# Performance work log

Hardware: AMD Instinct MI355X
Metric: run time of the kernel (lower is better)

Reference implementation:

```python
import jax, jax.numpy as jnp
import numpy as np

LOG2 = float(np.log(2.0))

def ssp(x):
    # shifted softplus: log(0.5*exp(x) + 0.5)
    return jax.nn.softplus(x) - LOG2


def setup_inputs() -> dict:
    B, A, N = 8, 512, 64
    n_atom, n_spatial, n_filters = 256, 128, 256
    n_ang_feat = 2 * 2 * 2 * 8 * 2  # 2*n_zetas*2*n_angular*n_zetas = 128
    key = jax.random.key(0)
    ks = jax.random.split(key, 16)
    f32 = jnp.float32
    inp = {
        'x': jax.random.normal(ks[0], (B, A, n_atom), f32),
        'r_ij': jax.random.uniform(ks[1], (B, A, N), f32) * 6.0,  # some beyond cutoff=5
        'f_ij': jax.random.normal(ks[2], (B, A, N, n_spatial), f32),
        'G_i': jax.random.normal(ks[3], (B, A, n_ang_feat), f32),
        'neighbor_mask': jnp.ones((B, A, N), f32),
        'neighbors': jax.random.randint(ks[4], (B, A, N), 0, A),
        # CFConv params: in2f (no bias), filter MLP, f2out
        'W_in2f': jax.random.normal(ks[5], (n_atom, n_filters), f32) * (n_atom ** -0.5),
        'W1': jax.random.normal(ks[6], (n_spatial, n_filters), f32) * (n_spatial ** -0.5),
        'b1': jnp.zeros((n_filters,), f32),
        'W2': jax.random.normal(ks[7], (n_filters, n_filters), f32) * (n_filters ** -0.5),
        'b2': jnp.zeros((n_filters,), f32),
        'W_f2out': jax.random.normal(ks[8], (n_filters, n_atom), f32) * (n_filters ** -0.5),
        'b_f2out': jnp.zeros((n_atom,), f32),
        # post-cfconv dense and angular dense (no bias)
        'W_dense': jax.random.normal(ks[9], (n_atom, n_atom), f32) * (n_atom ** -0.5),
        'b_dense': jnp.zeros((n_atom,), f32),
        'W_ang': jax.random.normal(ks[10], (n_ang_feat, n_atom), f32) * (n_ang_feat ** -0.5),
    }
    return inp


def reference(x, r_ij, f_ij, G_i, neighbor_mask, neighbors,
              W_in2f, W1, b1, W2, b2, W_f2out, b_f2out,
              W_dense, b_dense, W_ang):
    cutoff = 5.0
    # filter-generating MLP on distance expansion: [B,A,N,n_filters]
    W = ssp(jnp.einsum('bans,sf->banf', f_ij, W1) + b1)
    W = jnp.einsum('banf,fg->bang', W, W2) + b2
    # hard cutoff mask on distances
    C = (r_ij <= cutoff).astype(W.dtype)
    W = W * C[..., None]
    # in2f projection then neighbor gather
    xf = jnp.einsum('bad,df->baf', x, W_in2f)  # [B,A,F]
    B, A, F = xf.shape
    N = neighbors.shape[-1]
    y = jnp.take_along_axis(xf, neighbors.reshape(B, A * N, 1), axis=1)
    y = y.reshape(B, A, N, F)
    # elementwise filter, mask padded neighbors, sum-aggregate over neighbors
    y = (y * W * neighbor_mask[..., None]).sum(axis=2)  # [B,A,F]
    v_rad = jnp.einsum('baf,fd->bad', y, W_f2out) + b_f2out
    v_rad = jnp.einsum('bad,de->bae', v_rad, W_dense) + b_dense
    v_ang = jnp.einsum('bag,gd->bad', G_i, W_ang)
    return ssp(v_rad + v_ang)
```

## Files before the change

kernel.cpp:

```cpp
#include <hip/hip_runtime.h>


typedef __bf16 bf16x8 __attribute__((ext_vector_type(8)));
typedef float f32x4 __attribute__((ext_vector_type(4)));
typedef unsigned short u16;
typedef unsigned int u32;

#define LDA 136
#define LDH 264

__device__ __forceinline__ float b2f(u16 u) {
  union { float f; u32 i; } v; v.i = ((u32)u) << 16; return v.f;
}
__device__ __forceinline__ u32 rndb(float f) {
  u32 u = __builtin_bit_cast(u32, f);
  return u + 0x7fffu + ((u >> 16) & 1u);
}
__device__ __forceinline__ u16 f2b(float f) { return (u16)(rndb(f) >> 16); }
__device__ __forceinline__ u32 pkbf(float lo, float hi) {
  return __builtin_amdgcn_perm(rndb(hi), rndb(lo), 0x07060302);
}
__device__ __forceinline__ float sspf(float x) {
  float t = __expf(-fabsf(x));
  return fmaxf(x, 0.0f) + __logf(1.0f + t) - 0.6931471805599453f;
}
__device__ __forceinline__ bf16x8 ldfrag(const u16* p) {
  return __builtin_bit_cast(bf16x8, *(const uint4*)p);
}
__device__ __forceinline__ float ldsc(const u16* p, bool fm, size_t i) {
  return fm ? ((const float*)p)[i] : b2f(p[i]);
}
__device__ __forceinline__ void cvt8_store(u16* dst, const float* s) {
  float4 a = *(const float4*)s, b = *(const float4*)(s + 4);
  uint4 r;
  r.x = pkbf(a.x, a.y); r.y = pkbf(a.z, a.w);
  r.z = pkbf(b.x, b.y); r.w = pkbf(b.z, b.w);
  *(uint4*)dst = r;
}
__device__ __forceinline__ bf16x8 ldfragW_bf(const u16* W, int k0, int col, int quad) {
  union { u16 s[8]; bf16x8 v; } r;
#pragma unroll
  for (int j = 0; j < 8; j++) r.s[j] = W[(size_t)(k0 + quad * 8 + j) * 256 + col];
  return r.v;
}

__device__ __forceinline__ void pack_chunk(const u16* W, bool fm, int ksh, int idx, u16* dst) {
  int flane = idx & 63;
  int q = (idx >> 6) & ((1 << ksh) - 1);
  int c = idx >> (6 + ksh);
  int row = q * 32 + (flane >> 4) * 8;
  int col = c * 16 + (flane & 15);
  uint4 r;
  if (fm) {
    const float* p = (const float*)W + (size_t)row * 256 + col;
    r.x = pkbf(p[0], p[256]);   r.y = pkbf(p[512], p[768]);
    r.z = pkbf(p[1024], p[1280]); r.w = pkbf(p[1536], p[1792]);
  } else {
    const u16* p = W + (size_t)row * 256 + col;
    r.x = (u32)p[0] | ((u32)p[256] << 16);
    r.y = (u32)p[512] | ((u32)p[768] << 16);
    r.z = (u32)p[1024] | ((u32)p[1280] << 16);
    r.w = (u32)p[1536] | ((u32)p[1792] << 16);
  }
  *(uint4*)(dst + (size_t)idx * 8) = r;
}

__global__ __launch_bounds__(256) void pack_win(
    const u16* __restrict__ Win, const u16* __restrict__ nm, u16* __restrict__ outb) {
  if (nm[0] != 0) return;
  int g = blockIdx.x * 256 + threadIdx.x;
  pack_chunk(Win, true, 3, g, outb + 1048576);
}

__global__ __launch_bounds__(256) void pack5(
    const u16* __restrict__ W1, const u16* __restrict__ W2, const u16* __restrict__ Wf,
    const u16* __restrict__ Wd, const u16* __restrict__ Wa,
    const u16* __restrict__ nm, u16* __restrict__ dst) {
  bool fm = (nm[0] == 0);
  int g = blockIdx.x * 256 + threadIdx.x;
  if (g < 4096)        pack_chunk(W1, fm, 2, g, dst);
  else if (g < 12288)  pack_chunk(W2, fm, 3, g - 4096, dst + 32768);
  else if (g < 20480)  pack_chunk(Wf, fm, 3, g - 12288, dst + 98304);
  else if (g < 28672)  pack_chunk(Wd, fm, 3, g - 20480, dst + 163840);
  else                 pack_chunk(Wa, fm, 2, g - 28672, dst + 229376);
}

__global__ __launch_bounds__(256) void k1_xf(
    const u16* __restrict__ x, const u16* __restrict__ Win,
    const u16* __restrict__ nm, u16* __restrict__ outb) {
  __shared__ __align__(16) u16 sX[16 * LDH];
  bool fm = (nm[0] == 0);
  int bid = blockIdx.x, tid = threadIdx.x;
  int w = tid >> 6, lane = tid & 63, quad = lane >> 4, l16 = lane & 15;
  if (fm) {
    const float* src = (const float*)x + (size_t)bid * 4096;
#pragma unroll
    for (int i = 0; i < 2; i++) {
      int c = tid + 256 * i;
      cvt8_store(sX + (c >> 5) * LDH + (c & 31) * 8, src + c * 8);
    }
  } else {
    const u16* src = x + (size_t)bid * 4096;
#pragma unroll
    for (int i = 0; i < 2; i++) {
      int c = tid + 256 * i;
      *(uint4*)(sX + (c >> 5) * LDH + (c & 31) * 8) = *(const uint4*)(src + c * 8);
    }
  }
  __syncthreads();
  const u16* winp = outb + 1048576;
  f32x4 acc[4];
#pragma unroll
  for (int ct = 0; ct < 4; ct++) acc[ct] = (f32x4){0.f, 0.f, 0.f, 0.f};
#pragma unroll
  for (int q = 0; q < 8; q++) {
    bf16x8 af = ldfrag(sX + l16 * LDH + q * 32 + quad * 8);
    bf16x8 bfr[4];
#pragma unroll
    for (int ct = 0; ct < 4; ct++)
      bfr[ct] = fm ? ldfrag(winp + ((size_t)((w * 4 + ct) * 8 + q) * 64 + lane) * 8)
                   : ldfragW_bf(Win, q * 32, (w * 4 + ct) * 16 + l16, quad);
#pragma unroll
    for (int ct = 0; ct < 4; ct++)
      acc[ct] = __builtin_amdgcn_mfma_f32_16x16x32_bf16(af, bfr[ct], acc[ct], 0, 0, 0);
  }
#pragma unroll
  for (int ct = 0; ct < 4; ct++) {
    int f = w * 64 + ct * 16 + l16;
#pragma unroll
    for (int r = 0; r < 4; r++)
      outb[(size_t)(bid * 16 + quad * 4 + r) * 256 + f] = f2b(acc[ct][r]);
  }
}

__global__ __launch_bounds__(256, 3) void k2_main(
    u16* __restrict__ fij, const u16* __restrict__ rij, const u16* __restrict__ nm,
    const int* __restrict__ nbr, const u16* __restrict__ b1, const u16* __restrict__ b2,
    const u16* __restrict__ packed, const u16* __restrict__ xf) {
  __shared__ __align__(16) u16 sF[64 * LDA];
  __shared__ __align__(16) u16 sH[64 * LDH];
  __shared__ float cm[64];
  __shared__ int nb[64];
  bool fm = (nm[0] == 0);
  const u16* w1p = packed;
  const u16* w2p = packed + 32768;
  int bid = blockIdx.x, tid = threadIdx.x;
  int w = tid >> 6, lane = tid & 63, quad = lane >> 4, l16 = lane & 15;

  if (fm) {
    const float* fsrc = (const float*)fij + (size_t)bid * 8192;
#pragma unroll
    for (int i = 0; i < 4; i++) {
      int c = tid + 256 * i;
      cvt8_store(sF + (c >> 4) * LDA + (c & 15) * 8, fsrc + c * 8);
    }
  } else {
    const u16* fsrc = fij + (size_t)bid * 8192;
#pragma unroll
    for (int i = 0; i < 4; i++) {
      int c = tid + 256 * i;
      *(uint4*)(sF + (c >> 4) * LDA + (c & 15) * 8) = *(const uint4*)(fsrc + c * 8);
    }
  }
  if (tid < 64) {
    float r = ldsc(rij, fm, (size_t)bid * 64 + tid);
    float m = ldsc(nm, fm, (size_t)bid * 64 + tid);
    cm[tid] = (r <= 5.0f) ? m : 0.0f;
    nb[tid] = nbr[bid * 64 + tid];
  }
  __syncthreads();

  int b_of = (bid >> 9) * 512;
  u32 xr[4][4][2];
#pragma unroll
  for (int mt = 0; mt < 4; mt++)
#pragma unroll
    for (int r = 0; r < 4; r++) {
      int m = mt * 16 + quad * 4 + r;
      const u16* src = xf + ((size_t)(b_of + nb[m])) * 256 + w * 64 + l16;
      u32 t0 = src[0], t1 = src[16], t2 = src[32], t3 = src[48];
      xr[mt][r][0] = t0 | (t1 << 16);
      xr[mt][r][1] = t2 | (t3 << 16);
    }

  f32x4 zero = {0.f, 0.f, 0.f, 0.f};
  f32x4 acc[4][4];
#pragma unroll
  for (int mt = 0; mt < 4; mt++)
#pragma unroll
    for (int ct = 0; ct < 4; ct++) acc[mt][ct] = zero;
#pragma unroll
  for (int q = 0; q < 4; q++) {
    bf16x8 af[4], bfr[4];
#pragma unroll
    for (int mt = 0; mt < 4; mt++)
      af[mt] = ldfrag(sF + (mt * 16 + l16) * LDA + q * 32 + quad * 8);
#pragma unroll
    for (int ct = 0; ct < 4; ct++)
      bfr[ct] = ldfrag(w1p + ((size_t)((w * 4 + ct) * 4 + q) * 64 + lane) * 8);
#pragma unroll
    for (int mt = 0; mt < 4; mt++)
#pragma unroll
      for (int ct = 0; ct < 4; ct++)
        acc[mt][ct] = __builtin_amdgcn_mfma_f32_16x16x32_bf16(af[mt], bfr[ct], acc[mt][ct], 0, 0, 0);
  }
#pragma unroll
  for (int ct = 0; ct < 4; ct++) {
    int f = w * 64 + ct * 16 + l16;
    float bb = ldsc(b1, fm, f);
#pragma unroll
    for (int mt = 0; mt < 4; mt++)
#pragma unroll
      for (int r = 0; r < 4; r++)
        sH[(mt * 16 + quad * 4 + r) * LDH + f] = f2b(sspf(acc[mt][ct][r] + bb));
  }
  __syncthreads();

  f32x4 acc2[4][4];
#pragma unroll
  for (int mt = 0; mt < 4; mt++)
#pragma unroll
    for (int ct = 0; ct < 4; ct++) acc2[mt][ct] = zero;
#pragma unroll
  for (int q = 0; q < 8; q++) {
    bf16x8 af[4], bfr[4];
#pragma unroll
    for (int mt = 0; mt < 4; mt++)
      af[mt] = ldfrag(sH + (mt * 16 + l16) * LDH + q * 32 + quad * 8);
#pragma unroll
    for (int ct = 0; ct < 4; ct++)
      bfr[ct] = ldfrag(w2p + ((size_t)((w * 4 + ct) * 8 + q) * 64 + lane) * 8);
#pragma unroll
    for (int mt = 0; mt < 4; mt++)
#pragma unroll
      for (int ct = 0; ct < 4; ct++)
        acc2[mt][ct] = __builtin_amdgcn_mfma_f32_16x16x32_bf16(af[mt], bfr[ct], acc2[mt][ct], 0, 0, 0);
  }

  float bb[4], sv[4];
#pragma unroll
  for (int ct = 0; ct < 4; ct++) {
    bb[ct] = ldsc(b2, fm, w * 64 + ct * 16 + l16);
    sv[ct] = 0.0f;
  }
#pragma unroll
  for (int mt = 0; mt < 4; mt++)
#pragma unroll
    for (int r = 0; r < 4; r++) {
      int m = mt * 16 + quad * 4 + r;
      float c = cm[m];
      float x0 = __builtin_bit_cast(float, xr[mt][r][0] << 16);
      float x1 = __builtin_bit_cast(float, xr[mt][r][0] & 0xffff0000u);
      float x2 = __builtin_bit_cast(float, xr[mt][r][1] << 16);
      float x3 = __builtin_bit_cast(float, xr[mt][r][1] & 0xffff0000u);
      sv[0] += (acc2[mt][0][r] + bb[0]) * (c * x0);
      sv[1] += (acc2[mt][1][r] + bb[1]) * (c * x1);
      sv[2] += (acc2[mt][2][r] + bb[2]) * (c * x2);
      sv[3] += (acc2[mt][3][r] + bb[3]) * (c * x3);
    }
  size_t yoff = (size_t)bid * (fm ? 16384 : 8192);
#pragma unroll
  for (int ct = 0; ct < 4; ct++) {
    float s = sv[ct];
    s += __shfl_xor(s, 16, 64);
    s += __shfl_xor(s, 32, 64);
    if (quad == 0) fij[yoff + w * 64 + ct * 16 + l16] = f2b(s);
  }
}

__global__ __launch_bounds__(256, 3) void k3_out(
    const u16* __restrict__ fij, const u16* __restrict__ G, const u16* __restrict__ bf2,
    const u16* __restrict__ bd, const u16* __restrict__ nm,
    const u16* __restrict__ packed, u16* __restrict__ outb) {
  __shared__ __align__(16) u16 sY[32 * LDH];
  __shared__ __align__(16) u16 sH2[32 * LDH];
  __shared__ __align__(16) u16 sG[32 * LDA];
  bool fm = (nm[0] == 0);
  const u16* wfp = packed + 98304;
  const u16* wdp = packed + 163840;
  const u16* wap = packed + 229376;
  int bid = blockIdx.x, tid = threadIdx.x;
  int w = tid >> 6, lane = tid & 63, quad = lane >> 4, l16 = lane & 15;
  size_t ystr = fm ? 16384 : 8192;
#pragma unroll
  for (int i = 0; i < 4; i++) {
    int c = tid + 256 * i;
    int row = c >> 5;
    const u16* src = fij + (size_t)(bid * 32 + row) * ystr + (c & 31) * 8;
    *(uint4*)(sY + row * LDH + (c & 31) * 8) = *(const uint4*)src;
  }
  if (fm) {
    const float* g32 = (const float*)G;
#pragma unroll
    for (int i = 0; i < 2; i++) {
      int c = tid + 256 * i;
      int row = c >> 4;
      cvt8_store(sG + row * LDA + (c & 15) * 8, g32 + (size_t)(bid * 32 + row) * 128 + (c & 15) * 8);
    }
  } else {
#pragma unroll
    for (int i = 0; i < 2; i++) {
      int c = tid + 256 * i;
      int row = c >> 4;
      *(uint4*)(sG + row * LDA + (c & 15) * 8) =
          *(const uint4*)(G + (size_t)(bid * 32 + row) * 128 + (c & 15) * 8);
    }
  }
  __syncthreads();
  f32x4 zero = {0.f, 0.f, 0.f, 0.f};
  f32x4 acc[2][4];
#pragma unroll
  for (int mt = 0; mt < 2; mt++)
#pragma unroll
    for (int ct = 0; ct < 4; ct++) acc[mt][ct] = zero;
#pragma unroll
  for (int q = 0; q < 8; q++) {
    bf16x8 af[2], bfr[4];
#pragma unroll
    for (int mt = 0; mt < 2; mt++)
      af[mt] = ldfrag(sY + (mt * 16 + l16) * LDH + q * 32 + quad * 8);
#pragma unroll
    for (int ct = 0; ct < 4; ct++)
      bfr[ct] = ldfrag(wfp + ((size_t)((w * 4 + ct) * 8 + q) * 64 + lane) * 8);
#pragma unroll
    for (int mt = 0; mt < 2; mt++)
#pragma unroll
      for (int ct = 0; ct < 4; ct++)
        acc[mt][ct] = __builtin_amdgcn_mfma_f32_16x16x32_bf16(af[mt], bfr[ct], acc[mt][ct], 0, 0, 0);
  }
#pragma unroll
  for (int ct = 0; ct < 4; ct++) {
    int f = w * 64 + ct * 16 + l16;
    float bb = ldsc(bf2, fm, f);
#pragma unroll
    for (int mt = 0; mt < 2; mt++)
#pragma unroll
      for (int r = 0; r < 4; r++)
        sH2[(mt * 16 + quad * 4 + r) * LDH + f] = f2b(acc[mt][ct][r] + bb);
  }
  __syncthreads();
#pragma unroll
  for (int mt = 0; mt < 2; mt++)
#pragma unroll
    for (int ct = 0; ct < 4; ct++) acc[mt][ct] = zero;
#pragma unroll
  for (int q = 0; q < 8; q++) {
    bf16x8 af[2], bfr[4];
#pragma unroll
    for (int mt = 0; mt < 2; mt++)
      af[mt] = ldfrag(sH2 + (mt * 16 + l16) * LDH + q * 32 + quad * 8);
#pragma unroll
    for (int ct = 0; ct < 4; ct++)
      bfr[ct] = ldfrag(wdp + ((size_t)((w * 4 + ct) * 8 + q) * 64 + lane) * 8);
#pragma unroll
    for (int mt = 0; mt < 2; mt++)
#pragma unroll
      for (int ct = 0; ct < 4; ct++)
        acc[mt][ct] = __builtin_amdgcn_mfma_f32_16x16x32_bf16(af[mt], bfr[ct], acc[mt][ct], 0, 0, 0);
  }
#pragma unroll
  for (int q = 0; q < 4; q++) {
    bf16x8 af[2], bfr[4];
#pragma unroll
    for (int mt = 0; mt < 2; mt++)
      af[mt] = ldfrag(sG + (mt * 16 + l16) * LDA + q * 32 + quad * 8);
#pragma unroll
    for (int ct = 0; ct < 4; ct++)
      bfr[ct] = ldfrag(wap + ((size_t)((w * 4 + ct) * 4 + q) * 64 + lane) * 8);
#pragma unroll
    for (int mt = 0; mt < 2; mt++)
#pragma unroll
      for (int ct = 0; ct < 4; ct++)
        acc[mt][ct] = __builtin_amdgcn_mfma_f32_16x16x32_bf16(af[mt], bfr[ct], acc[mt][ct], 0, 0, 0);
  }
  float* out32 = (float*)outb;
#pragma unroll
  for (int ct = 0; ct < 4; ct++) {
    int f = w * 64 + ct * 16 + l16;
    float bb = ldsc(bd, fm, f);
#pragma unroll
    for (int mt = 0; mt < 2; mt++)
#pragma unroll
      for (int r = 0; r < 4; r++) {
        int m = mt * 16 + quad * 4 + r;
        float v = sspf(acc[mt][ct][r] + bb);
        size_t idx = ((size_t)bid * 32 + m) * 256 + f;
        if (fm) out32[idx] = v; else outb[idx] = f2b(v);
      }
  }
}

extern "C" void kernel_launch(void* const* d_in, const int* in_sizes, int n_in,
                              void* d_out, int out_size, void* d_ws, size_t ws_size,
                              hipStream_t stream) {
  u16*       x    = (u16*)d_in[0];
  const u16* rij  = (const u16*)d_in[1];
  u16*       fij  = (u16*)d_in[2];
  const u16* Gi   = (const u16*)d_in[3];
  const u16* nmsk = (const u16*)d_in[4];
  const int* nbr  = (const int*)d_in[5];
  const u16* Win  = (const u16*)d_in[6];
  const u16* W1   = (const u16*)d_in[7];
  const u16* b1   = (const u16*)d_in[8];
  const u16* W2   = (const u16*)d_in[9];
  const u16* b2   = (const u16*)d_in[10];
  const u16* Wf   = (const u16*)d_in[11];
  const u16* bf2  = (const u16*)d_in[12];
  const u16* Wd   = (const u16*)d_in[13];
  const u16* bd   = (const u16*)d_in[14];
  const u16* Wa   = (const u16*)d_in[15];
  u16* out = (u16*)d_out;

  pack_win<<<32, 256, 0, stream>>>(Win, nmsk, out);
  k1_xf<<<256, 256, 0, stream>>>(x, Win, nmsk, out);
  pack5<<<128, 256, 0, stream>>>(W1, W2, Wf, Wd, Wa, nmsk, x);
  k2_main<<<4096, 256, 0, stream>>>(fij, rij, nmsk, nbr, b1, b2, x, out);
  k3_out<<<128, 256, 0, stream>>>(fij, Gi, bf2, bd, nmsk, x, out);
}
```

Baseline: 345.9 us.

## Load f_ij fragments directly from global, stage weight packing through LDS

```diff
diff --git a/kernel.cpp b/kernel.cpp
--- a/kernel.cpp
+++ b/kernel.cpp
@@ -9,85 +9,100 @@
 #define LDA 136
 #define LDH 264
 
-__device__ __forceinline__ float b2f(u16 u) {
+static __device__ __forceinline__ float b2f(u16 u) {
   union { float f; u32 i; } v; v.i = ((u32)u) << 16; return v.f;
 }
-__device__ __forceinline__ u32 rndb(float f) {
+static __device__ __forceinline__ u32 rndb(float f) {
   u32 u = __builtin_bit_cast(u32, f);
   return u + 0x7fffu + ((u >> 16) & 1u);
 }
-__device__ __forceinline__ u16 f2b(float f) { return (u16)(rndb(f) >> 16); }
-__device__ __forceinline__ u32 pkbf(float lo, float hi) {
+static __device__ __forceinline__ u16 f2b(float f) { return (u16)(rndb(f) >> 16); }
+static __device__ __forceinline__ u32 pk2(float lo, float hi) {
   return __builtin_amdgcn_perm(rndb(hi), rndb(lo), 0x07060302);
 }
-__device__ __forceinline__ float sspf(float x) {
+static __device__ __forceinline__ float sspf(float x) {
   float t = __expf(-fabsf(x));
   return fmaxf(x, 0.0f) + __logf(1.0f + t) - 0.6931471805599453f;
 }
-__device__ __forceinline__ bf16x8 ldfrag(const u16* p) {
+static __device__ __forceinline__ bf16x8 ldfrag(const u16* p) {
   return __builtin_bit_cast(bf16x8, *(const uint4*)p);
 }
-__device__ __forceinline__ float ldsc(const u16* p, bool fm, size_t i) {
+static __device__ __forceinline__ bf16x8 mkfrag(u32 a, u32 b, u32 c, u32 d) {
+  uint4 t; t.x = a; t.y = b; t.z = c; t.w = d;
+  return __builtin_bit_cast(bf16x8, t);
+}
+static __device__ __forceinline__ float ldsc(const u16* p, bool fm, size_t i) {
   return fm ? ((const float*)p)[i] : b2f(p[i]);
 }
-__device__ __forceinline__ void cvt8_store(u16* dst, const float* s) {
-  float4 a = *(const float4*)s, b = *(const float4*)(s + 4);
-  uint4 r;
-  r.x = pkbf(a.x, a.y); r.y = pkbf(a.z, a.w);
-  r.z = pkbf(b.x, b.y); r.w = pkbf(b.z, b.w);
-  *(uint4*)dst = r;
-}
-__device__ __forceinline__ bf16x8 ldfragW_bf(const u16* W, int k0, int col, int quad) {
-  union { u16 s[8]; bf16x8 v; } r;
-#pragma unroll
-  for (int j = 0; j < 8; j++) r.s[j] = W[(size_t)(k0 + quad * 8 + j) * 256 + col];
-  return r.v;
-}
-
-__device__ __forceinline__ void pack_chunk(const u16* W, bool fm, int ksh, int idx, u16* dst) {
-  int flane = idx & 63;
-  int q = (idx >> 6) & ((1 << ksh) - 1);
-  int c = idx >> (6 + ksh);
-  int row = q * 32 + (flane >> 4) * 8;
-  int col = c * 16 + (flane & 15);
-  uint4 r;
+static __device__ __forceinline__ bf16x8 ldA(const u16* t, bool fm, size_t e) {
   if (fm) {
-    const float* p = (const float*)W + (size_t)row * 256 + col;
-    r.x = pkbf(p[0], p[256]);   r.y = pkbf(p[512], p[768]);
-    r.z = pkbf(p[1024], p[1280]); r.w = pkbf(p[1536], p[1792]);
+    const float* p = (const float*)t + e;
+    float4 a = *(const float4*)p, b = *(const float4*)(p + 4);
+    return mkfrag(pk2(a.x, a.y), pk2(a.z, a.w), pk2(b.x, b.y), pk2(b.z, b.w));
+  }
+  return ldfrag(t + e);
+}
+
+static __device__ __forceinline__ void pack_strip(
+    const u16* __restrict__ W, bool fm, int q, int KC, u16* __restrict__ dst, u16* T) {
+  int tid = threadIdx.x;
+  if (fm) {
+    const float* src = (const float*)W + (size_t)q * 32 * 256;
+#pragma unroll
+    for (int i = 0; i < 8; i++) {
+      int c = tid + 256 * i;
+      int row = c >> 6, col4 = (c & 63) * 4;
+      float4 v = *(const float4*)(src + (size_t)row * 256 + col4);
+      uint2 o; o.x = pk2(v.x, v.y); o.y = pk2(v.z, v.w);
+      *(uint2*)(T + row * LDH + col4) = o;
+    }
   } else {
-    const u16* p = W + (size_t)row * 256 + col;
-    r.x = (u32)p[0] | ((u32)p[256] << 16);
-    r.y = (u32)p[512] | ((u32)p[768] << 16);
-    r.z = (u32)p[1024] | ((u32)p[1280] << 16);
-    r.w = (u32)p[1536] | ((u32)p[1792] << 16);
-  }
-  *(uint4*)(dst + (size_t)idx * 8) = r;
+    const u16* src = W + (size_t)q * 32 * 256;
+#pragma unroll
+    for (int i = 0; i < 8; i++) {
+      int c = tid + 256 * i;
+      int row = c >> 6, col4 = (c & 63) * 4;
+      *(uint2*)(T + row * LDH + col4) = *(const uint2*)(src + (size_t)row * 256 + col4);
+    }
+  }
+  __syncthreads();
+#pragma unroll
+  for (int i = 0; i < 4; i++) {
+    int idx = tid + 256 * i;
+    int flane = idx & 63, c = idx >> 6;
+    int col = c * 16 + (flane & 15);
+    int r0 = (flane >> 4) * 8;
+    u32 t0 = (u32)T[(r0 + 0) * LDH + col] | ((u32)T[(r0 + 1) * LDH + col] << 16);
+    u32 t1 = (u32)T[(r0 + 2) * LDH + col] | ((u32)T[(r0 + 3) * LDH + col] << 16);
+    u32 t2 = (u32)T[(r0 + 4) * LDH + col] | ((u32)T[(r0 + 5) * LDH + col] << 16);
+    u32 t3 = (u32)T[(r0 + 6) * LDH + col] | ((u32)T[(r0 + 7) * LDH + col] << 16);
+    uint4 o; o.x = t0; o.y = t1; o.z = t2; o.w = t3;
+    *(uint4*)(dst + ((size_t)(c * KC + q) * 64 + flane) * 8) = o;
+  }
 }
 
 __global__ __launch_bounds__(256) void pack_win(
     const u16* __restrict__ Win, const u16* __restrict__ nm, u16* __restrict__ outb) {
-  if (nm[0] != 0) return;
-  int g = blockIdx.x * 256 + threadIdx.x;
-  pack_chunk(Win, true, 3, g, outb + 1048576);
+  __shared__ __align__(16) u16 T[32 * LDH];
+  pack_strip(Win, nm[0] == 0, blockIdx.x, 8, outb + 1048576, T);
 }
 
 __global__ __launch_bounds__(256) void pack5(
     const u16* __restrict__ W1, const u16* __restrict__ W2, const u16* __restrict__ Wf,
     const u16* __restrict__ Wd, const u16* __restrict__ Wa,
     const u16* __restrict__ nm, u16* __restrict__ dst) {
+  __shared__ __align__(16) u16 T[32 * LDH];
   bool fm = (nm[0] == 0);
-  int g = blockIdx.x * 256 + threadIdx.x;
-  if (g < 4096)        pack_chunk(W1, fm, 2, g, dst);
-  else if (g < 12288)  pack_chunk(W2, fm, 3, g - 4096, dst + 32768);
-  else if (g < 20480)  pack_chunk(Wf, fm, 3, g - 12288, dst + 98304);
-  else if (g < 28672)  pack_chunk(Wd, fm, 3, g - 20480, dst + 163840);
-  else                 pack_chunk(Wa, fm, 2, g - 28672, dst + 229376);
+  int b = blockIdx.x;
+  if (b < 4)       pack_strip(W1, fm, b,      4, dst,          T);
+  else if (b < 12) pack_strip(W2, fm, b - 4,  8, dst + 32768,  T);
+  else if (b < 20) pack_strip(Wf, fm, b - 12, 8, dst + 98304,  T);
+  else if (b < 28) pack_strip(Wd, fm, b - 20, 8, dst + 163840, T);
+  else             pack_strip(Wa, fm, b - 28, 4, dst + 229376, T);
 }
 
 __global__ __launch_bounds__(256) void k1_xf(
-    const u16* __restrict__ x, const u16* __restrict__ Win,
-    const u16* __restrict__ nm, u16* __restrict__ outb) {
+    const u16* __restrict__ x, const u16* __restrict__ nm, u16* __restrict__ outb) {
   __shared__ __align__(16) u16 sX[16 * LDH];
   bool fm = (nm[0] == 0);
   int bid = blockIdx.x, tid = threadIdx.x;
@@ -97,7 +112,10 @@
 #pragma unroll
     for (int i = 0; i < 2; i++) {
       int c = tid + 256 * i;
-      cvt8_store(sX + (c >> 5) * LDH + (c & 31) * 8, src + c * 8);
+      float4 a = *(const float4*)(src + c * 8), b = *(const float4*)(src + c * 8 + 4);
+      uint4 o; o.x = pk2(a.x, a.y); o.y = pk2(a.z, a.w);
+      o.z = pk2(b.x, b.y); o.w = pk2(b.z, b.w);
+      *(uint4*)(sX + (c >> 5) * LDH + (c & 31) * 8) = o;
     }
   } else {
     const u16* src = x + (size_t)bid * 4096;
@@ -118,8 +136,7 @@
     bf16x8 bfr[4];
 #pragma unroll
     for (int ct = 0; ct < 4; ct++)
-      bfr[ct] = fm ? ldfrag(winp + ((size_t)((w * 4 + ct) * 8 + q) * 64 + lane) * 8)
-                   : ldfragW_bf(Win, q * 32, (w * 4 + ct) * 16 + l16, quad);
+      bfr[ct] = ldfrag(winp + ((size_t)((w * 4 + ct) * 8 + q) * 64 + lane) * 8);
 #pragma unroll
     for (int ct = 0; ct < 4; ct++)
       acc[ct] = __builtin_amdgcn_mfma_f32_16x16x32_bf16(af, bfr[ct], acc[ct], 0, 0, 0);
@@ -137,7 +154,6 @@
     u16* __restrict__ fij, const u16* __restrict__ rij, const u16* __restrict__ nm,
     const int* __restrict__ nbr, const u16* __restrict__ b1, const u16* __restrict__ b2,
     const u16* __restrict__ packed, const u16* __restrict__ xf) {
-  __shared__ __align__(16) u16 sF[64 * LDA];
   __shared__ __align__(16) u16 sH[64 * LDH];
   __shared__ float cm[64];
   __shared__ int nb[64];
@@ -147,117 +163,95 @@
   int bid = blockIdx.x, tid = threadIdx.x;
   int w = tid >> 6, lane = tid & 63, quad = lane >> 4, l16 = lane & 15;
 
-  if (fm) {
-    const float* fsrc = (const float*)fij + (size_t)bid * 8192;
-#pragma unroll
-    for (int i = 0; i < 4; i++) {
-      int c = tid + 256 * i;
-      cvt8_store(sF + (c >> 4) * LDA + (c & 15) * 8, fsrc + c * 8);
-    }
-  } else {
-    const u16* fsrc = fij + (size_t)bid * 8192;
-#pragma unroll
-    for (int i = 0; i < 4; i++) {
-      int c = tid + 256 * i;
-      *(uint4*)(sF + (c >> 4) * LDA + (c & 15) * 8) = *(const uint4*)(fsrc + c * 8);
-    }
-  }
   if (tid < 64) {
     float r = ldsc(rij, fm, (size_t)bid * 64 + tid);
     float m = ldsc(nm, fm, (size_t)bid * 64 + tid);
     cm[tid] = (r <= 5.0f) ? m : 0.0f;
     nb[tid] = nbr[bid * 64 + tid];
   }
+
+  size_t abase = (size_t)bid * 8192;
+  f32x4 zero = {0.f, 0.f, 0.f, 0.f};
+  f32x4 acc[4][4];
+#pragma unroll
+  for (int mt = 0; mt < 4; mt++)
+#pragma unroll
+    for (int ct = 0; ct < 4; ct++) acc[mt][ct] = zero;
+#pragma unroll 2
+  for (int q = 0; q < 4; q++) {
+    bf16x8 af[4], bfr[4];
+#pragma unroll
+    for (int mt = 0; mt < 4; mt++)
+      af[mt] = ldA(fij, fm, abase + (size_t)(mt * 16 + l16) * 128 + q * 32 + quad * 8);
+#pragma unroll
+    for (int ct = 0; ct < 4; ct++)
+      bfr[ct] = ldfrag(w1p + ((size_t)((w * 4 + ct) * 4 + q) * 64 + lane) * 8);
+#pragma unroll
+    for (int mt = 0; mt < 4; mt++)
+#pragma unroll
+      for (int ct = 0; ct < 4; ct++)
+        acc[mt][ct] = __builtin_amdgcn_mfma_f32_16x16x32_bf16(af[mt], bfr[ct], acc[mt][ct], 0, 0, 0);
+  }
+  float bb1[4];
+#pragma unroll
+  for (int ct = 0; ct < 4; ct++) bb1[ct] = ldsc(b1, fm, w * 64 + ct * 16 + l16);
+#pragma unroll
+  for (int ct = 0; ct < 4; ct++) {
+    int f = w * 64 + ct * 16 + l16;
+#pragma unroll
+    for (int mt = 0; mt < 4; mt++)
+#pragma unroll
+      for (int r = 0; r < 4; r++)
+        sH[(mt * 16 + quad * 4 + r) * LDH + f] = f2b(sspf(acc[mt][ct][r] + bb1[ct]));
+  }
   __syncthreads();
 
+  f32x4 acc2[4][4];
+#pragma unroll
+  for (int mt = 0; mt < 4; mt++)
+#pragma unroll
+    for (int ct = 0; ct < 4; ct++) acc2[mt][ct] = zero;
+#pragma unroll 2
+  for (int q = 0; q < 8; q++) {
+    bf16x8 af[4], bfr[4];
+#pragma unroll
+    for (int mt = 0; mt < 4; mt++)
+      af[mt] = ldfrag(sH + (mt * 16 + l16) * LDH + q * 32 + quad * 8);
+#pragma unroll
+    for (int ct = 0; ct < 4; ct++)
+      bfr[ct] = ldfrag(w2p + ((size_t)((w * 4 + ct) * 8 + q) * 64 + lane) * 8);
+#pragma unroll
+    for (int mt = 0; mt < 4; mt++)
+#pragma unroll
+      for (int ct = 0; ct < 4; ct++)
+        acc2[mt][ct] = __builtin_amdgcn_mfma_f32_16x16x32_bf16(af[mt], bfr[ct], acc2[mt][ct], 0, 0, 0);
+  }
+
   int b_of = (bid >> 9) * 512;
-  u32 xr[4][4][2];
-#pragma unroll
-  for (int mt = 0; mt < 4; mt++)
+  float bb2[4], sv[4];
+#pragma unroll
+  for (int ct = 0; ct < 4; ct++) {
+    bb2[ct] = ldsc(b2, fm, w * 64 + ct * 16 + l16);
+    sv[ct] = 0.0f;
+  }
+  const u16* xcol = xf + w * 64 + l16;
+#pragma unroll
+  for (int mt = 0; mt < 4; mt++) {
+    float xv[4][4], cv[4];
 #pragma unroll
     for (int r = 0; r < 4; r++) {
       int m = mt * 16 + quad * 4 + r;
-      const u16* src = xf + ((size_t)(b_of + nb[m])) * 256 + w * 64 + l16;
-      u32 t0 = src[0], t1 = src[16], t2 = src[32], t3 = src[48];
-      xr[mt][r][0] = t0 | (t1 << 16);
-      xr[mt][r][1] = t2 | (t3 << 16);
-    }
-
-  f32x4 zero = {0.f, 0.f, 0.f, 0.f};
-  f32x4 acc[4][4];
-#pragma unroll
-  for (int mt = 0; mt < 4; mt++)
-#pragma unroll
-    for (int ct = 0; ct < 4; ct++) acc[mt][ct] = zero;
-#pragma unroll
-  for (int q = 0; q < 4; q++) {
-    bf16x8 af[4], bfr[4];
-#pragma unroll
-    for (int mt = 0; mt < 4; mt++)
-      af[mt] = ldfrag(sF + (mt * 16 + l16) * LDA + q * 32 + quad * 8);
-#pragma unroll
-    for (int ct = 0; ct < 4; ct++)
-      bfr[ct] = ldfrag(w1p + ((size_t)((w * 4 + ct) * 4 + q) * 64 + lane) * 8);
-#pragma unroll
-    for (int mt = 0; mt < 4; mt++)
-#pragma unroll
-      for (int ct = 0; ct < 4; ct++)
-        acc[mt][ct] = __builtin_amdgcn_mfma_f32_16x16x32_bf16(af[mt], bfr[ct], acc[mt][ct], 0, 0, 0);
-  }
-#pragma unroll
-  for (int ct = 0; ct < 4; ct++) {
-    int f = w * 64 + ct * 16 + l16;
-    float bb = ldsc(b1, fm, f);
-#pragma unroll
-    for (int mt = 0; mt < 4; mt++)
-#pragma unroll
-      for (int r = 0; r < 4; r++)
-        sH[(mt * 16 + quad * 4 + r) * LDH + f] = f2b(sspf(acc[mt][ct][r] + bb));
-  }
-  __syncthreads();
-
-  f32x4 acc2[4][4];
-#pragma unroll
-  for (int mt = 0; mt < 4; mt++)
-#pragma unroll
-    for (int ct = 0; ct < 4; ct++) acc2[mt][ct] = zero;
-#pragma unroll
-  for (int q = 0; q < 8; q++) {
-    bf16x8 af[4], bfr[4];
-#pragma unroll
-    for (int mt = 0; mt < 4; mt++)
-      af[mt] = ldfrag(sH + (mt * 16 + l16) * LDH + q * 32 + quad * 8);
-#pragma unroll
-    for (int ct = 0; ct < 4; ct++)
-      bfr[ct] = ldfrag(w2p + ((size_t)((w * 4 + ct) * 8 + q) * 64 + lane) * 8);
-#pragma unroll
-    for (int mt = 0; mt < 4; mt++)
-#pragma unroll
-      for (int ct = 0; ct < 4; ct++)
-        acc2[mt][ct] = __builtin_amdgcn_mfma_f32_16x16x32_bf16(af[mt], bfr[ct], acc2[mt][ct], 0, 0, 0);
-  }
-
-  float bb[4], sv[4];
-#pragma unroll
-  for (int ct = 0; ct < 4; ct++) {
-    bb[ct] = ldsc(b2, fm, w * 64 + ct * 16 + l16);
-    sv[ct] = 0.0f;
-  }
-#pragma unroll
-  for (int mt = 0; mt < 4; mt++)
-#pragma unroll
-    for (int r = 0; r < 4; r++) {
-      int m = mt * 16 + quad * 4 + r;
-      float c = cm[m];
-      float x0 = __builtin_bit_cast(float, xr[mt][r][0] << 16);
-      float x1 = __builtin_bit_cast(float, xr[mt][r][0] & 0xffff0000u);
-      float x2 = __builtin_bit_cast(float, xr[mt][r][1] << 16);
-      float x3 = __builtin_bit_cast(float, xr[mt][r][1] & 0xffff0000u);
-      sv[0] += (acc2[mt][0][r] + bb[0]) * (c * x0);
-      sv[1] += (acc2[mt][1][r] + bb[1]) * (c * x1);
-      sv[2] += (acc2[mt][2][r] + bb[2]) * (c * x2);
-      sv[3] += (acc2[mt][3][r] + bb[3]) * (c * x3);
-    }
+      const u16* src = xcol + (size_t)(b_of + nb[m]) * 256;
+      cv[r] = cm[m];
+      xv[r][0] = b2f(src[0]);  xv[r][1] = b2f(src[16]);
+      xv[r][2] = b2f(src[32]); xv[r][3] = b2f(src[48]);
+    }
+#pragma unroll
+    for (int r = 0; r < 4; r++)
+#pragma unroll
+      for (int ct = 0; ct < 4; ct++)
+        sv[ct] += (acc2[mt][ct][r] + bb2[ct]) * (cv[r] * xv[r][ct]);
+  }
   size_t yoff = (size_t)bid * (fm ? 16384 : 8192);
 #pragma unroll
   for (int ct = 0; ct < 4; ct++) {
@@ -295,7 +289,11 @@
     for (int i = 0; i < 2; i++) {
       int c = tid + 256 * i;
       int row = c >> 4;
-      cvt8_store(sG + row * LDA + (c & 15) * 8, g32 + (size_t)(bid * 32 + row) * 128 + (c & 15) * 8);
+      const float* p = g32 + (size_t)(bid * 32 + row) * 128 + (c & 15) * 8;
+      float4 a = *(const float4*)p, b = *(const float4*)(p + 4);
+      uint4 o; o.x = pk2(a.x, a.y); o.y = pk2(a.z, a.w);
+      o.z = pk2(b.x, b.y); o.w = pk2(b.z, b.w);
+      *(uint4*)(sG + row * LDA + (c & 15) * 8) = o;
     }
   } else {
 #pragma unroll
@@ -411,9 +409,9 @@
   const u16* Wa   = (const u16*)d_in[15];
   u16* out = (u16*)d_out;
 
-  pack_win<<<32, 256, 0, stream>>>(Win, nmsk, out);
-  k1_xf<<<256, 256, 0, stream>>>(x, Win, nmsk, out);
-  pack5<<<128, 256, 0, stream>>>(W1, W2, Wf, Wd, Wa, nmsk, x);
+  pack_win<<<8, 256, 0, stream>>>(Win, nmsk, out);
+  k1_xf<<<256, 256, 0, stream>>>(x, nmsk, out);
+  pack5<<<32, 256, 0, stream>>>(W1, W2, Wf, Wd, Wa, nmsk, x);
   k2_main<<<4096, 256, 0, stream>>>(fij, rij, nmsk, nbr, b1, b2, x, out);
   k3_out<<<128, 256, 0, stream>>>(fij, Gi, bf2, bd, nmsk, x, out);
 }
```

New measurement: 362.7 us. 1.05x slower.
